# Kernel optimization log

Measured on AMD Instinct MI355X. Metric: run time of the kernel, lower is better.

Reference implementation:

```python
import jax, jax.numpy as jnp
import numpy as np

N_NODES = 100000
IN_DIM = 64
HID = 64
N_EDGES = 1600000
EPS = 1e-5
SLOPE = 0.01  # F.leaky_relu default


def _glorot(key, shape):
    fan_in, fan_out = shape[1], shape[0]
    lim = jnp.sqrt(6.0 / (fan_in + fan_out))
    return jax.random.uniform(key, shape, jnp.float32, -lim, lim)


def setup_inputs() -> dict:
    key = jax.random.key(0)
    ks = jax.random.split(key, 8)
    x = jax.random.normal(ks[0], (N_NODES, IN_DIM), jnp.float32)
    src = jax.random.randint(ks[1], (N_EDGES,), 0, N_NODES, jnp.int32)
    dst = jax.random.randint(ks[2], (N_EDGES,), 0, N_NODES, jnp.int32)
    edge_index = jnp.stack([src, dst])  # [2, E]
    return {
        "x": x,
        "edge_index": edge_index,
        "W_self1": _glorot(ks[3], (HID, IN_DIM)),
        "W_neigh1": _glorot(ks[4], (HID, IN_DIM)),
        "b1": jnp.zeros((HID,), jnp.float32),
        "gamma1": jnp.ones((HID,), jnp.float32),
        "beta1": jnp.zeros((HID,), jnp.float32),
        "W_self2": _glorot(ks[5], (HID, HID)),
        "W_neigh2": _glorot(ks[6], (HID, HID)),
        "b2": jnp.zeros((HID,), jnp.float32),
        "gamma2": jnp.ones((HID,), jnp.float32),
        "beta2": jnp.zeros((HID,), jnp.float32),
    }


def _sage_mean(h, src, dst, W_self, W_neigh, b):
    # neighbor mean aggregation: mean of src features at each dst node
    msg_sum = jax.ops.segment_sum(h[src], dst, num_segments=N_NODES)  # [N, d]
    deg = jax.ops.segment_sum(jnp.ones_like(dst, jnp.float32), dst, num_segments=N_NODES)
    h_neigh = msg_sum / jnp.maximum(deg, 1.0)[:, None]  # isolated nodes -> 0
    return h @ W_self.T + h_neigh @ W_neigh.T + b


def _bn(h, gamma, beta):
    mu = jnp.mean(h, axis=0)
    var = jnp.mean(jnp.square(h - mu), axis=0)
    return (h - mu) * jax.lax.rsqrt(var + EPS) * gamma + beta


def reference(x, edge_index, W_self1, W_neigh1, b1, gamma1, beta1,
              W_self2, W_neigh2, b2, gamma2, beta2):
    src, dst = edge_index[0], edge_index[1]
    h = _sage_mean(x, src, dst, W_self1, W_neigh1, b1)
    h = jax.nn.leaky_relu(_bn(h, gamma1, beta1), SLOPE)
    h = _sage_mean(h, src, dst, W_self2, W_neigh2, b2)
    h = jax.nn.leaky_relu(_bn(h, gamma2, beta2), SLOPE)
    return h
```

## Files before the change

### kernel.cpp

```cpp
#include <hip/hip_runtime.h>

#define EPS 1e-5f
#define SLOPE 0.01f

typedef short bf16x8 __attribute__((ext_vector_type(8)));
typedef float f32x4 __attribute__((ext_vector_type(4)));

static __device__ __forceinline__ unsigned short f2bf(float f) {
  unsigned u = __float_as_uint(f);
  unsigned r = (u + 0x7FFFu + ((u >> 16) & 1u)) >> 16;
  return (unsigned short)r;
}
#define BFLO(u) __uint_as_float((u) << 16)
#define BFHI(u) __uint_as_float((u) & 0xFFFF0000u)


__global__ __launch_bounds__(1024) void hist_cvt_kernel(
    const int* __restrict__ dst, int* __restrict__ hist, int E, int NB,
    int histBlocks, const float* __restrict__ x, unsigned short* __restrict__ xb,
    int total4) {
  extern __shared__ int lh[];
  if ((int)blockIdx.x < histBlocks) {
    for (int i = threadIdx.x; i < NB; i += blockDim.x) lh[i] = 0;
    __syncthreads();
    int E4 = E >> 2;
    int stride = histBlocks * blockDim.x;
    const int4* d4 = (const int4*)dst;
    for (int i = blockIdx.x * blockDim.x + threadIdx.x; i < E4; i += stride) {
      int4 d = d4[i];
      atomicAdd(&lh[((unsigned)d.x) >> 8], 1);
      atomicAdd(&lh[((unsigned)d.y) >> 8], 1);
      atomicAdd(&lh[((unsigned)d.z) >> 8], 1);
      atomicAdd(&lh[((unsigned)d.w) >> 8], 1);
    }
    if (blockIdx.x == 0) {
      for (int i = (E4 << 2) + threadIdx.x; i < E; i += blockDim.x)
        atomicAdd(&lh[((unsigned)dst[i]) >> 8], 1);
    }
    __syncthreads();
    for (int b = threadIdx.x; b < NB; b += blockDim.x)
      hist[(size_t)b * histBlocks + blockIdx.x] = lh[b];
  } else {
    int cb = blockIdx.x - histBlocks;
    int stride = (gridDim.x - histBlocks) * blockDim.x;
    for (int i = cb * blockDim.x + threadIdx.x; i < total4; i += stride) {
      float4 v = reinterpret_cast<const float4*>(x)[i];
      ushort4 o;
      o.x = f2bf(v.x); o.y = f2bf(v.y); o.z = f2bf(v.z); o.w = f2bf(v.w);
      reinterpret_cast<ushort4*>(xb)[i] = o;
    }
  }
}

__global__ void scan_blk(const int* in, int* out, int* bsum, int n) {
  __shared__ int s[256];
  int i = blockIdx.x * 256 + threadIdx.x;
  int v = (i < n) ? in[i] : 0;
  s[threadIdx.x] = v;
  __syncthreads();
  for (int off = 1; off < 256; off <<= 1) {
    int t = (threadIdx.x >= off) ? s[threadIdx.x - off] : 0;
    __syncthreads();
    s[threadIdx.x] += t;
    __syncthreads();
  }
  if (i < n) out[i] = s[threadIdx.x] - v;
  if (threadIdx.x == 255) bsum[blockIdx.x] = s[255];
}

__global__ void scan_top(int* bsum, int nb) {
  __shared__ int s[512];
  int tid = threadIdx.x;
  int v = (tid < nb) ? bsum[tid] : 0;
  s[tid] = v;
  __syncthreads();
  for (int off = 1; off < 512; off <<= 1) {
    int t = (tid >= off) ? s[tid - off] : 0;
    __syncthreads();
    s[tid] += t;
    __syncthreads();
  }
  if (tid < nb) bsum[tid] = s[tid] - v;
}

__global__ __launch_bounds__(1024) void scatter_kernel(
    const int* __restrict__ src, const int* __restrict__ dst,
    const int* __restrict__ histS, const int* __restrict__ bsum,
    unsigned* __restrict__ binned, int E, int NB) {
  extern __shared__ int cur[];
  for (int b = threadIdx.x; b < NB; b += blockDim.x)
    cur[b] = histS[(size_t)b * gridDim.x + blockIdx.x] + bsum[b];
  __syncthreads();
  int E4 = E >> 2;
  int stride = gridDim.x * blockDim.x;
  const int4* d4 = (const int4*)dst;
  const int4* s4 = (const int4*)src;
  for (int i = blockIdx.x * blockDim.x + threadIdx.x; i < E4; i += stride) {
    int4 d = d4[i];
    int4 s = s4[i];
    int b0 = ((unsigned)d.x) >> 8;
    binned[atomicAdd(&cur[b0], 1)] = (unsigned)s.x | (((unsigned)d.x & 255u) << 20);
    int b1 = ((unsigned)d.y) >> 8;
    binned[atomicAdd(&cur[b1], 1)] = (unsigned)s.y | (((unsigned)d.y & 255u) << 20);
    int b2 = ((unsigned)d.z) >> 8;
    binned[atomicAdd(&cur[b2], 1)] = (unsigned)s.z | (((unsigned)d.z & 255u) << 20);
    int b3 = ((unsigned)d.w) >> 8;
    binned[atomicAdd(&cur[b3], 1)] = (unsigned)s.w | (((unsigned)d.w & 255u) << 20);
  }
  if (blockIdx.x == 0) {
    for (int i = (E4 << 2) + threadIdx.x; i < E; i += blockDim.x) {
      int d = dst[i];
      int b = ((unsigned)d) >> 8;
      binned[atomicAdd(&cur[b], 1)] = (unsigned)src[i] | (((unsigned)d & 255u) << 20);
    }
  }
}

__global__ __launch_bounds__(256) void fine_kernel(
    const unsigned* __restrict__ binned, const int* __restrict__ histS,
    const int* __restrict__ bsum,
    int* __restrict__ degarr, int* __restrict__ pptr, int* __restrict__ col,
    int E, int NB, int NBLKB, int N) {
  __shared__ int ldeg[256];
  __shared__ int lcur[256];
  __shared__ int ss[256];
  int b = blockIdx.x;
  int tid = threadIdx.x;
  int seg_s = histS[(size_t)b * NBLKB] + bsum[b];
  int seg_e = (b + 1 < NB) ? (histS[(size_t)(b + 1) * NBLKB] + bsum[b + 1]) : E;
  int pbase = (seg_s + b * 1024 + 3) & ~3;
  ldeg[tid] = 0;
  __syncthreads();
  for (int i = seg_s + tid; i < seg_e; i += 256)
    atomicAdd(&ldeg[(binned[i] >> 20) & 255u], 1);
  __syncthreads();
  int d = ldeg[tid];
  int pd = (d + 3) & ~3;
  ss[tid] = pd;
  __syncthreads();
  for (int off = 1; off < 256; off <<= 1) {
    int t = (tid >= off) ? ss[tid - off] : 0;
    __syncthreads();
    ss[tid] += t;
    __syncthreads();
  }
  int pstart = pbase + ss[tid] - pd;
  lcur[tid] = pstart;
  int node = (b << 8) + tid;
  if (node < N) {
    degarr[node] = d;
    pptr[node] = pstart;
  }
  __syncthreads();
  for (int i = seg_s + tid; i < seg_e; i += 256) {
    unsigned v = binned[i];
    int pos = atomicAdd(&lcur[(v >> 20) & 255u], 1);
    col[pos] = (int)(v & 0xFFFFFu);
  }
  for (int k = d; k < pd; ++k) col[pstart + k] = N;
}


__global__ __launch_bounds__(256) void agg_kernel(
    const unsigned short* __restrict__ hb, const int* __restrict__ degarr,
    const int* __restrict__ pptr, const int* __restrict__ col,
    unsigned short* __restrict__ hm, int n) {
  int t = blockIdx.x * 256 + threadIdx.x;
  int node = t >> 3;
  int fo = (t & 7) * 8;
  if (node >= n) return;
  int deg = degarr[node];
  const int4* cp = reinterpret_cast<const int4*>(col + pptr[node]);
  int nit = (deg + 3) >> 2;
  float s0 = 0.f, s1 = 0.f, s2 = 0.f, s3 = 0.f;
  float s4 = 0.f, s5 = 0.f, s6 = 0.f, s7 = 0.f;
  for (int it = 0; it < nit; ++it) {
    int4 c = cp[it];
    uint4 u0 = *reinterpret_cast<const uint4*>(&hb[(size_t)c.x * 64 + fo]);
    uint4 u1 = *reinterpret_cast<const uint4*>(&hb[(size_t)c.y * 64 + fo]);
    uint4 u2 = *reinterpret_cast<const uint4*>(&hb[(size_t)c.z * 64 + fo]);
    uint4 u3 = *reinterpret_cast<const uint4*>(&hb[(size_t)c.w * 64 + fo]);
    s0 += BFLO(u0.x) + BFLO(u1.x) + BFLO(u2.x) + BFLO(u3.x);
    s1 += BFHI(u0.x) + BFHI(u1.x) + BFHI(u2.x) + BFHI(u3.x);
    s2 += BFLO(u0.y) + BFLO(u1.y) + BFLO(u2.y) + BFLO(u3.y);
    s3 += BFHI(u0.y) + BFHI(u1.y) + BFHI(u2.y) + BFHI(u3.y);
    s4 += BFLO(u0.z) + BFLO(u1.z) + BFLO(u2.z) + BFLO(u3.z);
    s5 += BFHI(u0.z) + BFHI(u1.z) + BFHI(u2.z) + BFHI(u3.z);
    s6 += BFLO(u0.w) + BFLO(u1.w) + BFLO(u2.w) + BFLO(u3.w);
    s7 += BFHI(u0.w) + BFHI(u1.w) + BFHI(u2.w) + BFHI(u3.w);
  }
  float inv = 1.0f / (float)(deg > 0 ? deg : 1);
  uint4 o;
  o.x = (unsigned)f2bf(s0 * inv) | ((unsigned)f2bf(s1 * inv) << 16);
  o.y = (unsigned)f2bf(s2 * inv) | ((unsigned)f2bf(s3 * inv) << 16);
  o.z = (unsigned)f2bf(s4 * inv) | ((unsigned)f2bf(s5 * inv) << 16);
  o.w = (unsigned)f2bf(s6 * inv) | ((unsigned)f2bf(s7 * inv) << 16);
  *reinterpret_cast<uint4*>(&hm[(size_t)node * 64 + fo]) = o;
}


__global__ __launch_bounds__(256) void gemm_stream(
    const unsigned short* __restrict__ A0,
    const unsigned short* __restrict__ A1,
    const float* __restrict__ Wself, const float* __restrict__ Wneigh,
    const float* __restrict__ bias,
    unsigned short* __restrict__ zb, float* __restrict__ partial, int n, int ntiles) {
  int tid = threadIdx.x;
  int lane = tid & 63;
  int w = tid >> 6;
  int l15 = lane & 15;
  int g = lane >> 4;

  bf16x8 B[4][4];
  #pragma unroll
  for (int t = 0; t < 4; ++t) {
    #pragma unroll
    for (int s = 0; s < 4; ++s) {
      const float* base = (s < 2 ? Wself : Wneigh) + (t * 16 + l15) * 64 + (s & 1) * 32 + g * 8;
      float4 w0 = *reinterpret_cast<const float4*>(base);
      float4 w1 = *reinterpret_cast<const float4*>(base + 4);
      bf16x8 b;
      b[0] = (short)f2bf(w0.x); b[1] = (short)f2bf(w0.y);
      b[2] = (short)f2bf(w0.z); b[3] = (short)f2bf(w0.w);
      b[4] = (short)f2bf(w1.x); b[5] = (short)f2bf(w1.y);
      b[6] = (short)f2bf(w1.z); b[7] = (short)f2bf(w1.w);
      B[t][s] = b;
    }
  }
  float bv[4];
  #pragma unroll
  for (int t = 0; t < 4; ++t) bv[t] = bias[t * 16 + l15];

  float ps[4] = {0.f, 0.f, 0.f, 0.f};
  float pq[4] = {0.f, 0.f, 0.f, 0.f};

  int nw = gridDim.x * 4;
  for (int tile = blockIdx.x * 4 + w; tile < ntiles; tile += nw) {
    int r0 = tile * 16 + l15;
    uint4 a[4];
    if (r0 < n) {
      const uint4* pa0 = reinterpret_cast<const uint4*>(A0 + (size_t)r0 * 64);
      const uint4* pa1 = reinterpret_cast<const uint4*>(A1 + (size_t)r0 * 64);
      a[0] = pa0[g]; a[1] = pa0[4 + g]; a[2] = pa1[g]; a[3] = pa1[4 + g];
    } else {
      a[0] = a[1] = a[2] = a[3] = make_uint4(0u, 0u, 0u, 0u);
    }
    f32x4 acc[4] = {};
    #pragma unroll
    for (int s = 0; s < 4; ++s) {
      bf16x8 af = *reinterpret_cast<bf16x8*>(&a[s]);
      #pragma unroll
      for (int t = 0; t < 4; ++t)
        acc[t] = __builtin_amdgcn_mfma_f32_16x16x32_bf16(af, B[t][s], acc[t], 0, 0, 0);
    }
    #pragma unroll
    for (int t = 0; t < 4; ++t) {
      #pragma unroll
      for (int i = 0; i < 4; ++i) {
        int gr = tile * 16 + g * 4 + i;
        if (gr < n) {
          float v = acc[t][i] + bv[t];
          zb[(size_t)gr * 64 + t * 16 + l15] = f2bf(v);
          ps[t] += v;
          pq[t] += v * v;
        }
      }
    }
  }

  #pragma unroll
  for (int t = 0; t < 4; ++t) {
    ps[t] += __shfl_xor(ps[t], 16); ps[t] += __shfl_xor(ps[t], 32);
    pq[t] += __shfl_xor(pq[t], 16); pq[t] += __shfl_xor(pq[t], 32);
  }
  __shared__ float sred[128];
  if (tid < 128) sred[tid] = 0.f;
  __syncthreads();
  if (lane < 16) {
    #pragma unroll
    for (int t = 0; t < 4; ++t) {
      atomicAdd(&sred[t * 16 + l15], ps[t]);
      atomicAdd(&sred[64 + t * 16 + l15], pq[t]);
    }
  }
  __syncthreads();
  if (tid < 128) partial[(size_t)blockIdx.x * 128 + tid] = sred[tid];
}

__global__ __launch_bounds__(256) void reduce_coef(
    const float* __restrict__ partial, const float* __restrict__ gamma,
    const float* __restrict__ beta, float* __restrict__ coef, int nblk, float invN) {
  int f = blockIdx.x;
  float s = 0.f, q = 0.f;
  for (int j = threadIdx.x; j < nblk; j += 256) {
    s += partial[(size_t)j * 128 + f];
    q += partial[(size_t)j * 128 + 64 + f];
  }
  #pragma unroll
  for (int o = 1; o < 64; o <<= 1) {
    s += __shfl_xor(s, o);
    q += __shfl_xor(q, o);
  }
  __shared__ float rs[4], rq[4];
  if ((threadIdx.x & 63) == 0) {
    rs[threadIdx.x >> 6] = s;
    rq[threadIdx.x >> 6] = q;
  }
  __syncthreads();
  if (threadIdx.x == 0) {
    float S = rs[0] + rs[1] + rs[2] + rs[3];
    float Q = rq[0] + rq[1] + rq[2] + rq[3];
    float mu = S * invN;
    float var = Q * invN - mu * mu;
    float sc = rsqrtf(var + EPS) * gamma[f];
    coef[f] = sc;
    coef[64 + f] = beta[f] - mu * sc;
  }
}


__global__ void bn_bf16_kernel(const unsigned short* __restrict__ zb,
                               const float* __restrict__ coef,
                               unsigned short* __restrict__ out, int n) {
  __shared__ float sc[64];
  __shared__ float sh[64];
  if (threadIdx.x < 64) {
    sc[threadIdx.x] = coef[threadIdx.x];
    sh[threadIdx.x] = coef[64 + threadIdx.x];
  }
  __syncthreads();
  int total = n * 16;
  int stride = gridDim.x * blockDim.x;
  for (int idx = blockIdx.x * blockDim.x + threadIdx.x; idx < total; idx += stride) {
    int f0 = (idx & 15) * 4;
    uint2 u = reinterpret_cast<const uint2*>(zb)[idx];
    float t;
    ushort4 o;
    t = BFLO(u.x) * sc[f0 + 0] + sh[f0 + 0]; o.x = f2bf(t > 0.f ? t : SLOPE * t);
    t = BFHI(u.x) * sc[f0 + 1] + sh[f0 + 1]; o.y = f2bf(t > 0.f ? t : SLOPE * t);
    t = BFLO(u.y) * sc[f0 + 2] + sh[f0 + 2]; o.z = f2bf(t > 0.f ? t : SLOPE * t);
    t = BFHI(u.y) * sc[f0 + 3] + sh[f0 + 3]; o.w = f2bf(t > 0.f ? t : SLOPE * t);
    reinterpret_cast<ushort4*>(out)[idx] = o;
  }
}

__global__ void bn_f32_kernel(const unsigned short* __restrict__ zb,
                              const float* __restrict__ coef,
                              float* __restrict__ out, int n) {
  __shared__ float sc[64];
  __shared__ float sh[64];
  if (threadIdx.x < 64) {
    sc[threadIdx.x] = coef[threadIdx.x];
    sh[threadIdx.x] = coef[64 + threadIdx.x];
  }
  __syncthreads();
  int total = n * 16;
  int stride = gridDim.x * blockDim.x;
  for (int idx = blockIdx.x * blockDim.x + threadIdx.x; idx < total; idx += stride) {
    int f0 = (idx & 15) * 4;
    uint2 u = reinterpret_cast<const uint2*>(zb)[idx];
    float4 o;
    float t;
    t = BFLO(u.x) * sc[f0 + 0] + sh[f0 + 0]; o.x = t > 0.f ? t : SLOPE * t;
    t = BFHI(u.x) * sc[f0 + 1] + sh[f0 + 1]; o.y = t > 0.f ? t : SLOPE * t;
    t = BFLO(u.y) * sc[f0 + 2] + sh[f0 + 2]; o.z = t > 0.f ? t : SLOPE * t;
    t = BFHI(u.y) * sc[f0 + 3] + sh[f0 + 3]; o.w = t > 0.f ? t : SLOPE * t;
    reinterpret_cast<float4*>(out)[idx] = o;
  }
}


extern "C" void kernel_launch(void* const* d_in, const int* in_sizes, int n_in,
                              void* d_out, int out_size, void* d_ws, size_t ws_size,
                              hipStream_t stream) {
  const float* x  = (const float*)d_in[0];
  const int* ei   = (const int*)d_in[1];
  const float* Ws1 = (const float*)d_in[2];
  const float* Wn1 = (const float*)d_in[3];
  const float* b1  = (const float*)d_in[4];
  const float* g1  = (const float*)d_in[5];
  const float* be1 = (const float*)d_in[6];
  const float* Ws2 = (const float*)d_in[7];
  const float* Wn2 = (const float*)d_in[8];
  const float* b2  = (const float*)d_in[9];
  const float* g2  = (const float*)d_in[10];
  const float* be2 = (const float*)d_in[11];
  float* out = (float*)d_out;

  int N = in_sizes[0] / 64;
  int E = in_sizes[1] / 2;
  const int* src = ei;
  const int* dst = ei + E;

  int NB = (N + 255) >> 8;
  const int NBLKB = 256;
  int M = NB * NBLKB;

  int ntiles = (N + 15) / 16;
  int gblk = (ntiles + 7) / 8;

  char* ws = (char*)d_ws;
  float* coef1 = (float*)ws;
  float* coef2 = coef1 + 128;
  size_t off = 1024;
  auto take = [&](size_t bytes) {
    void* p = ws + off;
    off = (off + bytes + 255) & ~(size_t)255;
    return p;
  };
  int* hist   = (int*)take((size_t)M * 4);
  int* bsum   = (int*)take(512 * 4);
  int* degarr = (int*)take((size_t)N * 4);
  int* pptr   = (int*)take((size_t)N * 4);
  unsigned* binned = (unsigned*)take((size_t)E * 4);
  int* col    = (int*)take(((size_t)E + (size_t)NB * 1024 + 1024) * 4);
  unsigned short* xb  = (unsigned short*)take((size_t)(N + 1) * 64 * 2);
  unsigned short* hmb = (unsigned short*)take((size_t)N * 64 * 2);
  unsigned short* h1b = (unsigned short*)take((size_t)(N + 1) * 64 * 2);
  unsigned short* zb  = (unsigned short*)take((size_t)N * 64 * 2);
  float* partial = (float*)take((size_t)gblk * 128 * 4);

  hipMemsetAsync(xb + (size_t)N * 64, 0, 128, stream);
  hipMemsetAsync(h1b + (size_t)N * 64, 0, 128, stream);

  hist_cvt_kernel<<<NBLKB + 128, 1024, NB * 4, stream>>>(dst, hist, E, NB, NBLKB,
                                                         x, xb, N * 16);
  int nb1 = (M + 255) / 256;
  scan_blk<<<nb1, 256, 0, stream>>>(hist, hist, bsum, M);
  scan_top<<<1, 512, 0, stream>>>(bsum, nb1);
  scatter_kernel<<<NBLKB, 1024, NB * 4, stream>>>(src, dst, hist, bsum, binned, E, NB);
  fine_kernel<<<NB, 256, 0, stream>>>(binned, hist, bsum, degarr, pptr, col,
                                      E, NB, NBLKB, N);

  int ab = (N * 8 + 255) / 256;
  float invN = 1.0f / (float)N;

  agg_kernel<<<ab, 256, 0, stream>>>(xb, degarr, pptr, col, hmb, N);
  gemm_stream<<<gblk, 256, 0, stream>>>(xb, hmb, Ws1, Wn1, b1, zb, partial, N, ntiles);
  reduce_coef<<<64, 256, 0, stream>>>(partial, g1, be1, coef1, gblk, invN);
  bn_bf16_kernel<<<2048, 256, 0, stream>>>(zb, coef1, h1b, N);

  agg_kernel<<<ab, 256, 0, stream>>>(h1b, degarr, pptr, col, hmb, N);
  gemm_stream<<<gblk, 256, 0, stream>>>(h1b, hmb, Ws2, Wn2, b2, zb, partial, N, ntiles);
  reduce_coef<<<64, 256, 0, stream>>>(partial, g2, be2, coef2, gblk, invN);
  bn_f32_kernel<<<2048, 256, 0, stream>>>(zb, coef2, out, N);
}
```

Before: 180.6 us.

## Sort nodes by degree bucket to balance aggregation wavefronts

```diff
diff --git a/kernel.cpp b/kernel.cpp
--- a/kernel.cpp
+++ b/kernel.cpp
@@ -18,7 +18,7 @@
 __global__ __launch_bounds__(1024) void hist_cvt_kernel(
     const int* __restrict__ dst, int* __restrict__ hist, int E, int NB,
     int histBlocks, const float* __restrict__ x, unsigned short* __restrict__ xb,
-    int total4) {
+    unsigned short* __restrict__ h1b, int* __restrict__ nitcnt, int total4) {
   extern __shared__ int lh[];
   if ((int)blockIdx.x < histBlocks) {
     for (int i = threadIdx.x; i < NB; i += blockDim.x) lh[i] = 0;
@@ -42,8 +42,15 @@
       hist[(size_t)b * histBlocks + blockIdx.x] = lh[b];
   } else {
     int cb = blockIdx.x - histBlocks;
+    int tid = threadIdx.x;
+    if (cb == 0) {
+      ushort4 z4 = make_ushort4(0, 0, 0, 0);
+      if (tid < 64) nitcnt[tid] = 0;
+      else if (tid < 80) reinterpret_cast<ushort4*>(xb)[total4 + tid - 64] = z4;
+      else if (tid < 96) reinterpret_cast<ushort4*>(h1b)[total4 + tid - 80] = z4;
+    }
     int stride = (gridDim.x - histBlocks) * blockDim.x;
-    for (int i = cb * blockDim.x + threadIdx.x; i < total4; i += stride) {
+    for (int i = cb * blockDim.x + tid; i < total4; i += stride) {
       float4 v = reinterpret_cast<const float4*>(x)[i];
       ushort4 o;
       o.x = f2bf(v.x); o.y = f2bf(v.y); o.z = f2bf(v.z); o.w = f2bf(v.w);
@@ -120,16 +127,18 @@
     const unsigned* __restrict__ binned, const int* __restrict__ histS,
     const int* __restrict__ bsum,
     int* __restrict__ degarr, int* __restrict__ pptr, int* __restrict__ col,
-    int E, int NB, int NBLKB, int N) {
+    int* __restrict__ nitcnt, int E, int NB, int NBLKB, int N) {
   __shared__ int ldeg[256];
   __shared__ int lcur[256];
   __shared__ int ss[256];
+  __shared__ int nh[64];
   int b = blockIdx.x;
   int tid = threadIdx.x;
   int seg_s = histS[(size_t)b * NBLKB] + bsum[b];
   int seg_e = (b + 1 < NB) ? (histS[(size_t)(b + 1) * NBLKB] + bsum[b + 1]) : E;
   int pbase = (seg_s + b * 1024 + 3) & ~3;
   ldeg[tid] = 0;
+  if (tid < 64) nh[tid] = 0;
   __syncthreads();
   for (int i = seg_s + tid; i < seg_e; i += 256)
     atomicAdd(&ldeg[(binned[i] >> 20) & 255u], 1);
@@ -150,8 +159,10 @@
   if (node < N) {
     degarr[node] = d;
     pptr[node] = pstart;
-  }
-  __syncthreads();
+    atomicAdd(&nh[min(pd >> 2, 63)], 1);
+  }
+  __syncthreads();
+  if (tid < 64 && nh[tid]) atomicAdd(&nitcnt[tid], nh[tid]);
   for (int i = seg_s + tid; i < seg_e; i += 256) {
     unsigned v = binned[i];
     int pos = atomicAdd(&lcur[(v >> 20) & 255u], 1);
@@ -160,15 +171,51 @@
   for (int k = d; k < pd; ++k) col[pstart + k] = N;
 }
 
+__global__ void nit_scan(const int* __restrict__ nitcnt, int* __restrict__ nitcur) {
+  int tid = threadIdx.x;
+  int v = nitcnt[tid];
+  int x = v;
+  #pragma unroll
+  for (int o = 1; o < 64; o <<= 1) {
+    int y = __shfl_up(x, o);
+    if (tid >= o) x += y;
+  }
+  nitcur[tid] = x - v;
+}
+
+__global__ __launch_bounds__(1024) void perm_kernel(
+    const int* __restrict__ degarr, int* __restrict__ nitcur,
+    int* __restrict__ perm, int N) {
+  __shared__ int lh[64];
+  __shared__ int lc[64];
+  int tid = threadIdx.x;
+  if (tid < 64) lh[tid] = 0;
+  __syncthreads();
+  int node = blockIdx.x * 1024 + tid;
+  int bkt = 0;
+  if (node < N) {
+    bkt = min((degarr[node] + 3) >> 2, 63);
+    atomicAdd(&lh[bkt], 1);
+  }
+  __syncthreads();
+  if (tid < 64) lc[tid] = lh[tid] ? atomicAdd(&nitcur[tid], lh[tid]) : 0;
+  __syncthreads();
+  if (node < N) {
+    int pos = atomicAdd(&lc[bkt], 1);
+    perm[pos] = node;
+  }
+}
+
 
 __global__ __launch_bounds__(256) void agg_kernel(
     const unsigned short* __restrict__ hb, const int* __restrict__ degarr,
     const int* __restrict__ pptr, const int* __restrict__ col,
-    unsigned short* __restrict__ hm, int n) {
+    const int* __restrict__ perm, unsigned short* __restrict__ hm, int n) {
   int t = blockIdx.x * 256 + threadIdx.x;
-  int node = t >> 3;
+  int idx = t >> 3;
   int fo = (t & 7) * 8;
-  if (node >= n) return;
+  if (idx >= n) return;
+  int node = perm[idx];
   int deg = degarr[node];
   const int4* cp = reinterpret_cast<const int4*>(col + pptr[node]);
   int nit = (deg + 3) >> 2;
@@ -412,6 +459,9 @@
   int* bsum   = (int*)take(512 * 4);
   int* degarr = (int*)take((size_t)N * 4);
   int* pptr   = (int*)take((size_t)N * 4);
+  int* nitcnt = (int*)take(64 * 4);
+  int* nitcur = (int*)take(64 * 4);
+  int* perm   = (int*)take((size_t)N * 4);
   unsigned* binned = (unsigned*)take((size_t)E * 4);
   int* col    = (int*)take(((size_t)E + (size_t)NB * 1024 + 1024) * 4);
   unsigned short* xb  = (unsigned short*)take((size_t)(N + 1) * 64 * 2);
@@ -420,27 +470,26 @@
   unsigned short* zb  = (unsigned short*)take((size_t)N * 64 * 2);
   float* partial = (float*)take((size_t)gblk * 128 * 4);
 
-  hipMemsetAsync(xb + (size_t)N * 64, 0, 128, stream);
-  hipMemsetAsync(h1b + (size_t)N * 64, 0, 128, stream);
-
   hist_cvt_kernel<<<NBLKB + 128, 1024, NB * 4, stream>>>(dst, hist, E, NB, NBLKB,
-                                                         x, xb, N * 16);
+                                                         x, xb, h1b, nitcnt, N * 16);
   int nb1 = (M + 255) / 256;
   scan_blk<<<nb1, 256, 0, stream>>>(hist, hist, bsum, M);
   scan_top<<<1, 512, 0, stream>>>(bsum, nb1);
   scatter_kernel<<<NBLKB, 1024, NB * 4, stream>>>(src, dst, hist, bsum, binned, E, NB);
   fine_kernel<<<NB, 256, 0, stream>>>(binned, hist, bsum, degarr, pptr, col,
-                                      E, NB, NBLKB, N);
+                                      nitcnt, E, NB, NBLKB, N);
+  nit_scan<<<1, 64, 0, stream>>>(nitcnt, nitcur);
+  perm_kernel<<<(N + 1023) / 1024, 1024, 0, stream>>>(degarr, nitcur, perm, N);
 
   int ab = (N * 8 + 255) / 256;
   float invN = 1.0f / (float)N;
 
-  agg_kernel<<<ab, 256, 0, stream>>>(xb, degarr, pptr, col, hmb, N);
+  agg_kernel<<<ab, 256, 0, stream>>>(xb, degarr, pptr, col, perm, hmb, N);
   gemm_stream<<<gblk, 256, 0, stream>>>(xb, hmb, Ws1, Wn1, b1, zb, partial, N, ntiles);
   reduce_coef<<<64, 256, 0, stream>>>(partial, g1, be1, coef1, gblk, invN);
   bn_bf16_kernel<<<2048, 256, 0, stream>>>(zb, coef1, h1b, N);
 
-  agg_kernel<<<ab, 256, 0, stream>>>(h1b, degarr, pptr, col, hmb, N);
+  agg_kernel<<<ab, 256, 0, stream>>>(h1b, degarr, pptr, col, perm, hmb, N);
   gemm_stream<<<gblk, 256, 0, stream>>>(h1b, hmb, Ws2, Wn2, b2, zb, partial, N, ntiles);
   reduce_coef<<<64, 256, 0, stream>>>(partial, g2, be2, coef2, gblk, invN);
   bn_f32_kernel<<<2048, 256, 0, stream>>>(zb, coef2, out, N);
```

New measurement: 184.5 us. +2.2%, slower.
